# Kernel optimization log

Hardware: AMD Instinct MI355X
Metric: run time of the kernel (lower is better)

## Reference

```python
import jax, jax.numpy as jnp
import numpy as np

B = 64          # graphs per batch
N = 131072      # total nodes (B * 2048)
E = 524288      # total edges
V = 32000       # embedding vocab
D_IN = 256      # embed.output_size
D = 128         # GCN hidden size


def setup_inputs() -> dict:
    key = jax.random.key(0)
    ks = jax.random.split(key, 9)
    return {
        "node_tokens": jax.random.randint(ks[0], (N,), 0, V),
        "edge_index": jax.random.randint(ks[1], (2, E), 0, N),
        "embed_table": jax.random.normal(ks[2], (V, D_IN), jnp.float32),
        "W_node_w": jax.random.normal(ks[3], (D, D_IN), jnp.float32) * 0.02,
        "W_node_b": jax.random.normal(ks[4], (D,), jnp.float32) * 0.02,
        "conv1_w": jax.random.normal(ks[5], (D, D), jnp.float32) * 0.02,
        "conv1_b": jax.random.normal(ks[6], (D,), jnp.float32) * 0.02,
        "conv2_w": jax.random.normal(ks[7], (D, D), jnp.float32) * 0.02,
        "conv2_b": jax.random.normal(ks[8], (D,), jnp.float32) * 0.02,
    }


def _gcn_conv(x, src, dst, norm, W, b):
    # PyG GCNConv: linear first, then normalized scatter-add aggregation, then bias.
    x = x @ W.T                                        # [N, D]
    msg = x[src] * norm[:, None]                       # gather + per-edge scale
    out = jax.ops.segment_sum(msg, dst, num_segments=N)  # scatter-add at dst
    return out + b


def reference(node_tokens, edge_index, embed_table, W_node_w, W_node_b,
              conv1_w, conv1_b, conv2_w, conv2_b):
    # compute_node_features: embed lookup -> W_node linear (no mask path)
    x = embed_table[node_tokens] @ W_node_w.T + W_node_b   # [N, D]

    # GCNConv normalization with self-loops (shared by both layers)
    loop = jnp.arange(N)
    src = jnp.concatenate([edge_index[0], loop])
    dst = jnp.concatenate([edge_index[1], loop])
    deg = jax.ops.segment_sum(jnp.ones(E + N, x.dtype), dst, num_segments=N)
    dinv = jnp.where(deg > 0, jax.lax.rsqrt(deg), 0.0)
    norm = dinv[src] * dinv[dst]                           # [E+N]

    x = jax.nn.relu(_gcn_conv(x, src, dst, norm, conv1_w, conv1_b))
    x = _gcn_conv(x, src, dst, norm, conv2_w, conv2_b)

    # Unpad into [B, max_n, D]; equal-length graphs, no edge tokens -> reshape.
    n = N // B
    output = x.reshape(B, n, D)          # dropout_p=0 -> identity
    labels = node_tokens.reshape(B, n)
    labels_mask = jnp.ones((B, n), dtype=bool)
    label_node_ids = jnp.broadcast_to(jnp.arange(n), (B, n))
    return output, labels, labels_mask, label_node_ids
```

## Files before the change

kernel.cpp:

```cpp
#include <hip/hip_runtime.h>
#include <hip/hip_bf16.h>

#define N_NODES 131072
#define N_EDGES 524288
#define DHID    128
#define DIN     256
#define VOCAB   32000

typedef __attribute__((ext_vector_type(8))) short short8;
typedef __attribute__((ext_vector_type(4))) float floatx4;

__device__ inline short bf16_rne(float f) {
    union { float f; unsigned u; } v; v.f = f;
    unsigned r = v.u + 0x7FFF + ((v.u >> 16) & 1);
    return (short)(r >> 16);
}
__device__ inline float bf16_to_f(short s) {
    union { unsigned u; float f; } v; v.u = ((unsigned)(unsigned short)s) << 16;
    return v.f;
}
__device__ inline short8 cvt8(float4 lo, float4 hi) {
    short8 o;
    o[0] = bf16_rne(lo.x); o[1] = bf16_rne(lo.y);
    o[2] = bf16_rne(lo.z); o[3] = bf16_rne(lo.w);
    o[4] = bf16_rne(hi.x); o[5] = bf16_rne(hi.y);
    o[6] = bf16_rne(hi.z); o[7] = bf16_rne(hi.w);
    return o;
}


#define MEGA_VB 250
#define MEGA_WB 128
#define MEGA_TOTAL (MEGA_VB + MEGA_WB + N_EDGES / 256)

__global__ __launch_bounds__(256) void mega(const float* __restrict__ emb,
                                            const float* __restrict__ Wn,
                                            short* __restrict__ z,
                                            const float* __restrict__ W1,
                                            const float* __restrict__ W2,
                                            short* __restrict__ W1b,
                                            short* __restrict__ W2b,
                                            const int* __restrict__ edst,
                                            int* __restrict__ counts) {
    const int b = blockIdx.x;
    if (b < MEGA_VB) {
        const int t = threadIdx.x;
        const int wid  = t >> 6;
        const int lane = t & 63;
        const int col  = lane & 15;
        const int quad = lane >> 4;
        const int vbase = b * 128 + wid * 32;
        const size_t row0 = (size_t)(vbase + col);
        const size_t row1 = (size_t)(vbase + 16 + col);

        floatx4 acc[2][8] = {};
#pragma unroll
        for (int kc = 0; kc < DIN / 32; ++kc) {
            const int ko = kc * 32 + quad * 8;
            short8 a0 = cvt8(*(const float4*)&emb[row0 * DIN + ko],
                             *(const float4*)&emb[row0 * DIN + ko + 4]);
            short8 a1 = cvt8(*(const float4*)&emb[row1 * DIN + ko],
                             *(const float4*)&emb[row1 * DIN + ko + 4]);
#pragma unroll
            for (int ft = 0; ft < 8; ++ft) {
                const size_t wr = (size_t)(col * 8 + ft) * DIN + ko;
                short8 bb = cvt8(*(const float4*)&Wn[wr],
                                 *(const float4*)&Wn[wr + 4]);
                acc[0][ft] = __builtin_amdgcn_mfma_f32_16x16x32_bf16(a0, bb, acc[0][ft], 0, 0, 0);
                acc[1][ft] = __builtin_amdgcn_mfma_f32_16x16x32_bf16(a1, bb, acc[1][ft], 0, 0, 0);
            }
        }
#pragma unroll
        for (int mt = 0; mt < 2; ++mt) {
#pragma unroll
            for (int r = 0; r < 4; ++r) {
                const int row = vbase + mt * 16 + quad * 4 + r;
                short8 o;
#pragma unroll
                for (int ft = 0; ft < 8; ++ft)
                    o[ft] = bf16_rne(acc[mt][ft][r]);
                *(short8*)&z[(size_t)row * DHID + col * 8] = o;
            }
        }
    } else if (b < MEGA_VB + MEGA_WB) {
        int i = (b - MEGA_VB) * 256 + threadIdx.x;
        if (i < 16384) W1b[i] = bf16_rne(W1[i]);
        else           W2b[i - 16384] = bf16_rne(W2[i - 16384]);
    } else {
        int e = (b - MEGA_VB - MEGA_WB) * 256 + threadIdx.x;
        atomicAdd(&counts[edst[e]], 1);
    }
}


__global__ __launch_bounds__(256) void alloc_csr(const int* __restrict__ counts,
                                                 int* __restrict__ offsets,
                                                 int* __restrict__ cursor,
                                                 float* __restrict__ dinv,
                                                 int* __restrict__ total,
                                                 const int* __restrict__ tok,
                                                 float* __restrict__ meta_out) {
    __shared__ int s[256];
    __shared__ int base;
    int i = blockIdx.x * 256 + threadIdx.x;
    int v = counts[i];
    s[threadIdx.x] = v;
    __syncthreads();
    for (int d = 1; d < 256; d <<= 1) {
        int t = (threadIdx.x >= d) ? s[threadIdx.x - d] : 0;
        __syncthreads();
        s[threadIdx.x] += t;
        __syncthreads();
    }
    int incl = s[threadIdx.x];
    if (threadIdx.x == 255) base = atomicAdd(total, incl);
    __syncthreads();
    int off = base + incl - v;
    offsets[i] = off;
    cursor[i]  = off;
    dinv[i] = rsqrtf((float)(v + 1));

    const size_t L0 = (size_t)N_NODES * DHID;
    meta_out[L0 + i]               = (float)tok[i];
    meta_out[L0 + N_NODES + i]     = 1.0f;
    meta_out[L0 + 2 * N_NODES + i] = (float)(i & 2047);
}

__global__ __launch_bounds__(256) void fill_csr(const int* __restrict__ src,
                                                const int* __restrict__ dst,
                                                int* __restrict__ cursor,
                                                const float* __restrict__ dinv,
                                                const int* __restrict__ tok,
                                                int4* __restrict__ csr) {
    int e = blockIdx.x * 256 + threadIdx.x;
    int d = dst[e];
    int s = src[e];
    int p = atomicAdd(&cursor[d], 1);
    csr[p] = make_int4(s, tok[s], __float_as_int(dinv[s]), 0);
}


template <bool RELU, bool OUT_BF16, bool ZG>
__global__ __launch_bounds__(256, 8) void fused_conv(const short* __restrict__ x,
                                                     const int4* __restrict__ csr,
                                                     const int* __restrict__ offsets,
                                                     const int* __restrict__ counts,
                                                     const float* __restrict__ dinv,
                                                     const int* __restrict__ tok,
                                                     const float* __restrict__ bn,
                                                     const short* __restrict__ Wb,
                                                     const float* __restrict__ bias,
                                                     void* __restrict__ outp) {
    const int t = threadIdx.x;
    const int wid  = t >> 6;
    const int lane = t & 63;
    const int col  = lane & 15;
    const int quad = lane >> 4;
    const int base = (blockIdx.x * 4 + wid) * 16;
    const int node = base + col;

    const float di = dinv[node];
    const int beg = offsets[node];
    const int cnt = counts[node];
    const int4* pcsr = csr + beg;

    float af[4][8];
    {
        const int self = ZG ? tok[node] : node;
        const size_t xrow = (size_t)self * DHID + quad * 8;
#pragma unroll
        for (int c = 0; c < 4; ++c) {
            short8 v = *(const short8*)&x[xrow + c * 32];
#pragma unroll
            for (int j = 0; j < 8; ++j) af[c][j] = di * bf16_to_f(v[j]);
        }
    }
    float sw = di;

    int4 cn = (cnt > 0) ? pcsr[0] : make_int4(0, 0, 0, 0);
    for (int e = 0; e < cnt; ++e) {
        const int   s = ZG ? cn.y : cn.x;
        const float w = __int_as_float(cn.z);
        if (e + 1 < cnt) cn = pcsr[e + 1];
        if (ZG) sw += w;
        const size_t r0 = (size_t)s * DHID + quad * 8;
        short8 u0 = *(const short8*)&x[r0];
        short8 u1 = *(const short8*)&x[r0 + 32];
        short8 u2 = *(const short8*)&x[r0 + 64];
        short8 u3 = *(const short8*)&x[r0 + 96];
#pragma unroll
        for (int j = 0; j < 8; ++j) {
            af[0][j] = fmaf(w, bf16_to_f(u0[j]), af[0][j]);
            af[1][j] = fmaf(w, bf16_to_f(u1[j]), af[1][j]);
            af[2][j] = fmaf(w, bf16_to_f(u2[j]), af[2][j]);
            af[3][j] = fmaf(w, bf16_to_f(u3[j]), af[3][j]);
        }
    }

    short8 a[4];
#pragma unroll
    for (int c = 0; c < 4; ++c) {
        if (ZG) {
            const float4 b0 = *(const float4*)&bn[c * 32 + quad * 8];
            const float4 b1 = *(const float4*)&bn[c * 32 + quad * 8 + 4];
            const float bv[8] = {b0.x, b0.y, b0.z, b0.w, b1.x, b1.y, b1.z, b1.w};
#pragma unroll
            for (int j = 0; j < 8; ++j)
                a[c][j] = bf16_rne(di * (af[c][j] + sw * bv[j]));
        } else {
#pragma unroll
            for (int j = 0; j < 8; ++j) a[c][j] = bf16_rne(di * af[c][j]);
        }
    }

    floatx4 acc[8] = {};
#pragma unroll
    for (int c = 0; c < 4; ++c) {
        const int ko = c * 32 + quad * 8;
#pragma unroll
        for (int ft = 0; ft < 8; ++ft) {
            short8 b = *(const short8*)&Wb[(size_t)(col * 8 + ft) * DHID + ko];
            acc[ft] = __builtin_amdgcn_mfma_f32_16x16x32_bf16(a[c], b, acc[ft], 0, 0, 0);
        }
    }

    const float4 bv0 = *(const float4*)&bias[col * 8];
    const float4 bv1 = *(const float4*)&bias[col * 8 + 4];
    const float bb[8] = {bv0.x, bv0.y, bv0.z, bv0.w, bv1.x, bv1.y, bv1.z, bv1.w};
    short* outb = (short*)outp;
    float* outf = (float*)outp;
#pragma unroll
    for (int r = 0; r < 4; ++r) {
        const size_t row = (size_t)(base + quad * 4 + r) * DHID + col * 8;
        if (OUT_BF16) {
            short8 o;
#pragma unroll
            for (int ft = 0; ft < 8; ++ft) {
                float v = acc[ft][r] + bb[ft];
                if (RELU) v = fmaxf(v, 0.f);
                o[ft] = bf16_rne(v);
            }
            *(short8*)&outb[row] = o;
        } else {
            float4 o0, o1;
            o0.x = acc[0][r] + bb[0]; o0.y = acc[1][r] + bb[1];
            o0.z = acc[2][r] + bb[2]; o0.w = acc[3][r] + bb[3];
            o1.x = acc[4][r] + bb[4]; o1.y = acc[5][r] + bb[5];
            o1.z = acc[6][r] + bb[6]; o1.w = acc[7][r] + bb[7];
            if (RELU) {
                o0.x = fmaxf(o0.x, 0.f); o0.y = fmaxf(o0.y, 0.f);
                o0.z = fmaxf(o0.z, 0.f); o0.w = fmaxf(o0.w, 0.f);
                o1.x = fmaxf(o1.x, 0.f); o1.y = fmaxf(o1.y, 0.f);
                o1.z = fmaxf(o1.z, 0.f); o1.w = fmaxf(o1.w, 0.f);
            }
            *(float4*)&outf[row] = o0;
            *(float4*)&outf[row + 4] = o1;
        }
    }
}


extern "C" void kernel_launch(void* const* d_in, const int* in_sizes, int n_in,
                              void* d_out, int out_size, void* d_ws, size_t ws_size,
                              hipStream_t stream) {
    const int*   tok  = (const int*)d_in[0];
    const int*   esrc = (const int*)d_in[1];
    const int*   edst = esrc + N_EDGES;
    const float* emb  = (const float*)d_in[2];
    const float* Wn   = (const float*)d_in[3];
    const float* bn   = (const float*)d_in[4];
    const float* W1   = (const float*)d_in[5];
    const float* b1   = (const float*)d_in[6];
    const float* W2   = (const float*)d_in[7];
    const float* b2   = (const float*)d_in[8];
    float* out = (float*)d_out;

    char* ws = (char*)d_ws;
    int*   counts  = (int*)(ws);
    int*   total   = (int*)(ws + (1u << 19));
    int*   offsets = (int*)(ws + (1u << 19) + 256);
    int*   cursor  = (int*)(ws + (2u << 19) + 256);
    float* dinv    = (float*)(ws + (3u << 19) + 256);
    int4*  csr     = (int4*)(ws + 3 * (1u << 20));
    short* W1b     = (short*)(ws + 11 * (1u << 20));
    short* W2b     = (short*)(ws + 11 * (1u << 20) + (1u << 15));
    short* z       = (short*)(ws + 12 * (1u << 20));
    short* x2b     = (short*)(ws + 24 * (1u << 20));

    hipMemsetAsync(counts, 0, (1u << 19) + 256, stream);
    mega<<<MEGA_TOTAL, 256, 0, stream>>>(emb, Wn, z, W1, W2, W1b, W2b, edst, counts);
    alloc_csr<<<N_NODES / 256, 256, 0, stream>>>(counts, offsets, cursor, dinv,
                                                 total, tok, out);
    fill_csr<<<N_EDGES / 256, 256, 0, stream>>>(esrc, edst, cursor, dinv, tok, csr);

    fused_conv<true, true, true><<<N_NODES / 64, 256, 0, stream>>>(
        z, csr, offsets, counts, dinv, tok, bn, W1b, b1, x2b);
    fused_conv<false, false, false><<<N_NODES / 64, 256, 0, stream>>>(
        x2b, csr, offsets, counts, dinv, tok, bn, W2b, b2, out);
}
```

Before: 286.8 us.

## Pack CSR entries into 32-bit words and recompute edge weights from degree

```diff
diff --git a/kernel.cpp b/kernel.cpp
--- a/kernel.cpp
+++ b/kernel.cpp
@@ -121,28 +121,32 @@
     dinv[i] = rsqrtf((float)(v + 1));
 
     const size_t L0 = (size_t)N_NODES * DHID;
-    meta_out[L0 + i]               = (float)tok[i];
-    meta_out[L0 + N_NODES + i]     = 1.0f;
-    meta_out[L0 + 2 * N_NODES + i] = (float)(i & 2047);
-}
+    __builtin_nontemporal_store((float)tok[i],     &meta_out[L0 + i]);
+    __builtin_nontemporal_store(1.0f,              &meta_out[L0 + N_NODES + i]);
+    __builtin_nontemporal_store((float)(i & 2047), &meta_out[L0 + 2 * N_NODES + i]);
+}
+
 
 __global__ __launch_bounds__(256) void fill_csr(const int* __restrict__ src,
                                                 const int* __restrict__ dst,
                                                 int* __restrict__ cursor,
-                                                const float* __restrict__ dinv,
+                                                const int* __restrict__ counts,
                                                 const int* __restrict__ tok,
-                                                int4* __restrict__ csr) {
+                                                int* __restrict__ csr1,
+                                                int* __restrict__ csr2) {
     int e = blockIdx.x * 256 + threadIdx.x;
     int d = dst[e];
     int s = src[e];
     int p = atomicAdd(&cursor[d], 1);
-    csr[p] = make_int4(s, tok[s], __float_as_int(dinv[s]), 0);
+    int deg = counts[s];
+    csr1[p] = (deg << 24) | tok[s];
+    csr2[p] = (deg << 24) | s;
 }
 
 
 template <bool RELU, bool OUT_BF16, bool ZG>
 __global__ __launch_bounds__(256, 8) void fused_conv(const short* __restrict__ x,
-                                                     const int4* __restrict__ csr,
+                                                     const int* __restrict__ csr,
                                                      const int* __restrict__ offsets,
                                                      const int* __restrict__ counts,
                                                      const float* __restrict__ dinv,
@@ -162,7 +166,7 @@
     const float di = dinv[node];
     const int beg = offsets[node];
     const int cnt = counts[node];
-    const int4* pcsr = csr + beg;
+    const int* pcsr = csr + beg;
 
     float af[4][8];
     {
@@ -177,10 +181,10 @@
     }
     float sw = di;
 
-    int4 cn = (cnt > 0) ? pcsr[0] : make_int4(0, 0, 0, 0);
+    int cn = (cnt > 0) ? pcsr[0] : 0;
     for (int e = 0; e < cnt; ++e) {
-        const int   s = ZG ? cn.y : cn.x;
-        const float w = __int_as_float(cn.z);
+        const int   s = cn & 0xFFFFFF;
+        const float w = rsqrtf((float)(((unsigned)cn >> 24) + 1));
         if (e + 1 < cnt) cn = pcsr[e + 1];
         if (ZG) sw += w;
         const size_t r0 = (size_t)s * DHID + quad * 8;
@@ -242,19 +246,20 @@
             }
             *(short8*)&outb[row] = o;
         } else {
-            float4 o0, o1;
-            o0.x = acc[0][r] + bb[0]; o0.y = acc[1][r] + bb[1];
-            o0.z = acc[2][r] + bb[2]; o0.w = acc[3][r] + bb[3];
-            o1.x = acc[4][r] + bb[4]; o1.y = acc[5][r] + bb[5];
-            o1.z = acc[6][r] + bb[6]; o1.w = acc[7][r] + bb[7];
+            floatx4 o0, o1;
+            o0[0] = acc[0][r] + bb[0]; o0[1] = acc[1][r] + bb[1];
+            o0[2] = acc[2][r] + bb[2]; o0[3] = acc[3][r] + bb[3];
+            o1[0] = acc[4][r] + bb[4]; o1[1] = acc[5][r] + bb[5];
+            o1[2] = acc[6][r] + bb[6]; o1[3] = acc[7][r] + bb[7];
             if (RELU) {
-                o0.x = fmaxf(o0.x, 0.f); o0.y = fmaxf(o0.y, 0.f);
-                o0.z = fmaxf(o0.z, 0.f); o0.w = fmaxf(o0.w, 0.f);
-                o1.x = fmaxf(o1.x, 0.f); o1.y = fmaxf(o1.y, 0.f);
-                o1.z = fmaxf(o1.z, 0.f); o1.w = fmaxf(o1.w, 0.f);
+#pragma unroll
+                for (int k = 0; k < 4; ++k) {
+                    o0[k] = fmaxf(o0[k], 0.f);
+                    o1[k] = fmaxf(o1[k], 0.f);
+                }
             }
-            *(float4*)&outf[row] = o0;
-            *(float4*)&outf[row + 4] = o1;
+            __builtin_nontemporal_store(o0, (floatx4*)&outf[row]);
+            __builtin_nontemporal_store(o1, (floatx4*)&outf[row + 4]);
         }
     }
 }
@@ -281,20 +286,22 @@
     int*   offsets = (int*)(ws + (1u << 19) + 256);
     int*   cursor  = (int*)(ws + (2u << 19) + 256);
     float* dinv    = (float*)(ws + (3u << 19) + 256);
-    int4*  csr     = (int4*)(ws + 3 * (1u << 20));
-    short* W1b     = (short*)(ws + 11 * (1u << 20));
-    short* W2b     = (short*)(ws + 11 * (1u << 20) + (1u << 15));
-    short* z       = (short*)(ws + 12 * (1u << 20));
-    short* x2b     = (short*)(ws + 24 * (1u << 20));
+    int*   csr1    = (int*)(ws + 3 * (1u << 20));
+    int*   csr2    = (int*)(ws + 5 * (1u << 20));
+    short* W1b     = (short*)(ws + 7 * (1u << 20));
+    short* W2b     = (short*)(ws + 7 * (1u << 20) + (1u << 15));
+    short* z       = (short*)(ws + 8 * (1u << 20));
+    short* x2b     = (short*)(ws + 16 * (1u << 20));
 
     hipMemsetAsync(counts, 0, (1u << 19) + 256, stream);
     mega<<<MEGA_TOTAL, 256, 0, stream>>>(emb, Wn, z, W1, W2, W1b, W2b, edst, counts);
     alloc_csr<<<N_NODES / 256, 256, 0, stream>>>(counts, offsets, cursor, dinv,
                                                  total, tok, out);
-    fill_csr<<<N_EDGES / 256, 256, 0, stream>>>(esrc, edst, cursor, dinv, tok, csr);
+    fill_csr<<<N_EDGES / 256, 256, 0, stream>>>(esrc, edst, cursor, counts, tok,
+                                                csr1, csr2);
 
     fused_conv<true, true, true><<<N_NODES / 64, 256, 0, stream>>>(
-        z, csr, offsets, counts, dinv, tok, bn, W1b, b1, x2b);
+        z, csr1, offsets, counts, dinv, tok, bn, W1b, b1, x2b);
     fused_conv<false, false, false><<<N_NODES / 64, 256, 0, stream>>>(
-        x2b, csr, offsets, counts, dinv, tok, bn, W2b, b2, out);
-}
+        x2b, csr2, offsets, counts, dinv, tok, bn, W2b, b2, out);
+}
```

New measurement: 294.5 us. +2.7%, slower.
